# Kernel optimization log

Measured on AMD Instinct MI355X. Metric: run time of the kernel, lower is better.

Reference implementation:

```python
import jax, jax.numpy as jnp
import numpy as np

DIM = 1024
N_HEADS = 16
HEAD_DIM = DIM // N_HEADS
COND_DIM = 1024
MLP_RATIO = 4
B = 8
L = 1024  # per-sequence length (equal lengths -> T = B*L packed tokens)
T = B * L
EPS = 1e-5


def setup_inputs() -> dict:
    key = jax.random.key(0)
    ks = jax.random.split(key, 16)
    s = 0.02
    # rotary tables: [max_pos, head_dim//2]
    inv_freq = 1.0 / (10000.0 ** (jnp.arange(0, HEAD_DIM, 2, dtype=jnp.float32) / HEAD_DIM))
    t = jnp.arange(L, dtype=jnp.float32)
    freqs = t[:, None] * inv_freq[None, :]  # [L, HEAD_DIM//2]
    return {
        "x": jax.random.normal(ks[0], (T, DIM), jnp.float32),
        "lengths": jnp.full((B,), L, dtype=jnp.int64),
        "offsets": jnp.arange(B, dtype=jnp.int64) * L,
        "cos": jnp.cos(freqs),
        "sin": jnp.sin(freqs),
        "positions": jnp.tile(jnp.arange(L, dtype=jnp.int64), B),
        "c": jax.random.normal(ks[1], (B, COND_DIM), jnp.float32),
        "ln1_w": jnp.ones((DIM,), jnp.float32),
        "Wq": jax.random.normal(ks[2], (DIM, DIM), jnp.float32) * s,
        "Wk": jax.random.normal(ks[3], (DIM, DIM), jnp.float32) * s,
        "Wv": jax.random.normal(ks[4], (DIM, DIM), jnp.float32) * s,
        "Wo": jax.random.normal(ks[5], (DIM, DIM), jnp.float32) * s,
        "ln2_w": jnp.ones((DIM,), jnp.float32),
        "W1": jax.random.normal(ks[6], (DIM, MLP_RATIO * DIM), jnp.float32) * s,
        "b1": jnp.zeros((MLP_RATIO * DIM,), jnp.float32),
        "W2": jax.random.normal(ks[7], (MLP_RATIO * DIM, DIM), jnp.float32) * s,
        "b2": jnp.zeros((DIM,), jnp.float32),
        "ada_w": jax.random.normal(ks[8], (COND_DIM, 6 * DIM), jnp.float32) * s,
        "ada_b": jnp.zeros((6 * DIM,), jnp.float32),
    }


def _layer_norm(x, w):
    # LayerNorm with weight only (no bias), as in the torch module
    mu = jnp.mean(x, axis=-1, keepdims=True)
    var = jnp.mean(jnp.square(x - mu), axis=-1, keepdims=True)
    return (x - mu) * jax.lax.rsqrt(var + EPS) * w


def _rope(q, k, cos, sin, positions):
    # q, k: [T, H, D]; cos/sin: [max_pos, D//2]; half-split RoPE
    c = cos[positions][:, None, :]  # [T, 1, D//2]
    s = sin[positions][:, None, :]
    def rot(x):
        x1, x2 = jnp.split(x, 2, axis=-1)
        return jnp.concatenate([x1 * c - x2 * s, x2 * c + x1 * s], axis=-1)
    return rot(q), rot(k)


def reference(x, lengths, offsets, cos, sin, positions, c,
              ln1_w, Wq, Wk, Wv, Wo, ln2_w, W1, b1, W2, b2, ada_w, ada_b):
    # adaLN modulation: [B, 6*DIM] -> six [B, DIM]
    ada = c @ ada_w + ada_b
    sh_msa, sc_msa, g_msa, sh_mlp, sc_mlp, g_mlp = jnp.split(ada, 6, axis=-1)
    # per-token gather via seq_ids (equal lengths -> repeat each row L times)
    seq_ids = jnp.repeat(jnp.arange(B), L)  # = repeat_interleave(arange(B), lengths)
    sh_msa_t, sc_msa_t, g_msa_t = sh_msa[seq_ids], sc_msa[seq_ids], g_msa[seq_ids]
    sh_mlp_t, sc_mlp_t, g_mlp_t = sh_mlp[seq_ids], sc_mlp[seq_ids], g_mlp[seq_ids]

    x_skip = x
    h = _layer_norm(x, ln1_w) * (1.0 + sc_msa_t) + sh_msa_t
    q = (h @ Wq).reshape(T, N_HEADS, HEAD_DIM)
    k = (h @ Wk).reshape(T, N_HEADS, HEAD_DIM)
    v = (h @ Wv).reshape(T, N_HEADS, HEAD_DIM)
    q, k = _rope(q, k, cos, sin, positions)

    # intra-sequence-only attention: with equal lengths the block-diagonal
    # score_mod mask is exactly per-sequence attention -> reshape to [B, L, H, D]
    qb = q.reshape(B, L, N_HEADS, HEAD_DIM)
    kb = k.reshape(B, L, N_HEADS, HEAD_DIM)
    vb = v.reshape(B, L, N_HEADS, HEAD_DIM)
    scores = jnp.einsum('blhd,bmhd->bhlm', qb, kb) / jnp.sqrt(jnp.float32(HEAD_DIM))
    probs = jax.nn.softmax(scores, axis=-1)
    attn = jnp.einsum('bhlm,bmhd->blhd', probs, vb).reshape(T, DIM)

    x = x_skip + g_msa_t * (attn @ Wo)  # dropout p is identity in eval mode

    h2 = _layer_norm(x, ln2_w) * (1.0 + sc_mlp_t) + sh_mlp_t
    mlp = jax.nn.gelu(h2 @ W1 + b1, approximate=True) @ W2 + b2
    return x + g_mlp_t * mlp
```

## Files before the change

### kernel.cpp

```cpp
#include <hip/hip_runtime.h>

typedef unsigned short u16;
typedef __attribute__((ext_vector_type(8))) short short8;
typedef __attribute__((ext_vector_type(4))) float f32x4;
typedef __attribute__((ext_vector_type(4))) unsigned uint4v;

__device__ __forceinline__ float bf2f(u16 u){
  unsigned v = ((unsigned)u) << 16;
  return __builtin_bit_cast(float, v);
}
__device__ __forceinline__ u16 f2bf(float f){
  unsigned u = __builtin_bit_cast(unsigned, f);
  u += 0x7fff + ((u >> 16) & 1);
  return (u16)(u >> 16);
}
__device__ __forceinline__ unsigned packbf(float lo, float hi){
  return ((unsigned)f2bf(hi) << 16) | (unsigned)f2bf(lo);
}
__device__ __forceinline__ void async16(const void* g, void* l){
  __builtin_amdgcn_global_load_lds((const __attribute__((address_space(1))) void*)g,
                                   (__attribute__((address_space(3))) void*)l, 16, 0, 0);
}

__global__ __launch_bounds__(256) void ada_partial(
    const float* __restrict__ c, const float* __restrict__ aw,
    float* __restrict__ part){
  int n  = blockIdx.x*256 + threadIdx.x;
  int b  = blockIdx.y;
  int kc = blockIdx.z;
  const float* cr  = c + b*1024 + kc*128;
  const float* awp = aw + (size_t)(kc*128)*6144 + n;
  float acc = 0.f;
#pragma unroll 8
  for (int k = 0; k < 128; ++k)
    acc += cr[k] * awp[(size_t)k*6144];
  part[(size_t)(kc*8 + b)*6144 + n] = acc;
}

__global__ __launch_bounds__(256) void ada_reduce(
    const float* __restrict__ part, const float* __restrict__ ab,
    float* __restrict__ ada){
  int idx = blockIdx.x*256 + threadIdx.x;
  int n = idx % 6144;
  float acc = ab[n];
#pragma unroll
  for (int kc = 0; kc < 8; ++kc)
    acc += part[(size_t)kc*49152 + idx];
  ada[idx] = acc;
}

__global__ __launch_bounds__(256) void transpose_cast(
    const float* __restrict__ src, u16* __restrict__ dst, int K, int N){
  __shared__ float t[64][65];
  int n0 = blockIdx.x*64, k0 = blockIdx.y*64;
  int tid = threadIdx.x;
  int cc = tid & 63, r4 = tid >> 6;
#pragma unroll 4
  for (int it = 0; it < 16; ++it){
    int r = it*4 + r4;
    t[r][cc] = src[(size_t)(k0 + r)*N + n0 + cc];
  }
  __syncthreads();
#pragma unroll 4
  for (int it = 0; it < 16; ++it){
    int r = it*4 + r4;
    dst[(size_t)(n0 + r)*K + k0 + cc] = f2bf(t[cc][r]);
  }
}

__global__ __launch_bounds__(256) void ln_mod(
    const float* __restrict__ x, u16* __restrict__ out,
    const float* __restrict__ w, const float* __restrict__ ada,
    int shift_off, int scale_off){
  int t = blockIdx.x, tid = threadIdx.x;
  const float* xr = x + (size_t)t*1024;
  float v[4]; float s = 0.f, ss = 0.f;
#pragma unroll
  for (int i = 0; i < 4; ++i){ v[i] = xr[tid + i*256]; s += v[i]; ss += v[i]*v[i]; }
  for (int d = 1; d < 64; d <<= 1){ s += __shfl_xor(s, d); ss += __shfl_xor(ss, d); }
  __shared__ float red[8];
  int wv = tid >> 6;
  if ((tid & 63) == 0){ red[wv] = s; red[4+wv] = ss; }
  __syncthreads();
  s = red[0]+red[1]+red[2]+red[3];
  ss = red[4]+red[5]+red[6]+red[7];
  float mu = s * (1.f/1024.f);
  float var = ss * (1.f/1024.f) - mu*mu;
  float rs = rsqrtf(var + 1e-5f);
  int b = t >> 10;
  const float* sh = ada + b*6144 + shift_off;
  const float* sc = ada + b*6144 + scale_off;
#pragma unroll
  for (int i = 0; i < 4; ++i){
    int cidx = tid + i*256;
    float hh = (v[i]-mu)*rs*w[cidx]*(1.f + sc[cidx]) + sh[cidx];
    out[(size_t)t*1024 + cidx] = f2bf(hh);
  }
}

template<int EPI>
__global__ __launch_bounds__(256) void gemm_bt(
    const u16* __restrict__ A, const u16* __restrict__ Bt,
    void* __restrict__ Cout, int M, int N, int K, int m_off,
    const float* __restrict__ e0, const float* __restrict__ e1,
    const float* __restrict__ e2){
  __shared__ u16 As[128*32];
  __shared__ u16 Bs[128*32];
  const int tid = threadIdx.x;
  const int n0 = blockIdx.x*128, m0 = blockIdx.y*128;
  const int w = tid >> 6, lane = tid & 63, quad = lane >> 4, ln = lane & 15;
  const int wm = (w >> 1)*64, wn = (w & 1)*64;
  f32x4 acc[4][4] = {};
  const u16* ga = A  + (size_t)(m0 + (tid>>2))*K + (tid&3)*8;
  const u16* gb = Bt + (size_t)(n0 + (tid>>2))*K + (tid&3)*8;
  u16* lA = As + (tid & 192)*8;
  u16* lB = Bs + (tid & 192)*8;
  const size_t rstep = (size_t)64*K;
  for (int k0 = 0; k0 < K; k0 += 32){
    async16(ga,         lA);
    async16(ga + rstep, lA + 2048);
    async16(gb,         lB);
    async16(gb + rstep, lB + 2048);
    ga += 32; gb += 32;
    __syncthreads();
    short8 af[4], bfr[4];
#pragma unroll
    for (int i = 0; i < 4; ++i){
      af[i]  = *(const short8*)(As + (wm + i*16 + ln)*32 + quad*8);
      bfr[i] = *(const short8*)(Bs + (wn + i*16 + ln)*32 + quad*8);
    }
#pragma unroll
    for (int i = 0; i < 4; ++i)
#pragma unroll
      for (int j = 0; j < 4; ++j)
        acc[i][j] = __builtin_amdgcn_mfma_f32_16x16x32_bf16(af[i], bfr[j], acc[i][j], 0, 0, 0);
    __syncthreads();
  }
  const int mB = m0 + wm + quad*4;
  const int nB = n0 + wn + ln;
#pragma unroll
  for (int i = 0; i < 4; ++i){
#pragma unroll
    for (int r = 0; r < 4; ++r){
      const int m = mB + i*16 + r;
#pragma unroll
      for (int j = 0; j < 4; ++j){
        const int n = nB + j*16;
        float v = acc[i][j][r];
        if (EPI == 0){
          ((u16*)Cout)[(size_t)m*N + n] = f2bf(v);
        } else if (EPI == 1){
          const int b = (m + m_off) >> 10;
          float g = e1[b*6144 + 2048 + n];
          ((float*)Cout)[(size_t)m*N + n] = e0[(size_t)m*N + n] + g*v;
        } else if (EPI == 2){
          float xx = v + e0[n];
          float th = tanhf(0.7978845608f*(xx + 0.044715f*xx*xx*xx));
          ((u16*)Cout)[(size_t)m*N + n] = f2bf(0.5f*xx*(1.0f + th));
        } else {
          const int b = (m + m_off) >> 10;
          float g = e1[b*6144 + 5120 + n];
          ((float*)Cout)[(size_t)m*N + n] = e2[(size_t)m*N + n] + g*(v + e0[n]);
        }
      }
    }
  }
}

__global__ __launch_bounds__(256) void rope_pack(
    const u16* __restrict__ qkv, const float* __restrict__ cosT,
    const float* __restrict__ sinT, u16* __restrict__ qp,
    u16* __restrict__ kp, u16* __restrict__ vt){
  int blk = blockIdx.x;
  int lt = blk & 15, h = (blk >> 4) & 15, b = blk >> 8;
  int l0 = lt*64;
  int bh = b*16 + h;
  __shared__ u16 vl[64][68];
  int tid = threadIdx.x;
  size_t tile_base = (size_t)bh*65536 + (size_t)lt*4096;
#pragma unroll 4
  for (int it = 0; it < 16; ++it){
    int idx = it*256 + tid;
    int r = idx >> 6, d = idx & 63;
    int t = b*1024 + l0 + r;
    int pos = l0 + r;
    const u16* row = qkv + (size_t)t*3072 + h*64;
    float qv = bf2f(row[d]), kv = bf2f(row[1024+d]);
    float qo, ko;
    if (d < 32){
      float cs = cosT[pos*32 + d], sn = sinT[pos*32 + d];
      qo = qv*cs - bf2f(row[d+32])*sn;
      ko = kv*cs - bf2f(row[1024+d+32])*sn;
    } else {
      int dd = d - 32;
      float cs = cosT[pos*32 + dd], sn = sinT[pos*32 + dd];
      qo = qv*cs + bf2f(row[d-32])*sn;
      ko = kv*cs + bf2f(row[1024+d-32])*sn;
    }
    qp[((size_t)bh*1024 + l0 + r)*64 + d] = f2bf(qo*0.125f);
    kp[tile_base + (d>>5)*2048 + r*32 + (d&31)] = f2bf(ko);
    vl[d][r] = row[2048 + d];
  }
  __syncthreads();
#pragma unroll 4
  for (int it = 0; it < 16; ++it){
    int idx = it*256 + tid;
    int d = idx >> 6, cc = idx & 63;
    vt[tile_base + (cc>>5)*2048 + d*32 + (cc&31)] = vl[d][cc];
  }
}

__global__ __launch_bounds__(256) void attn_kernel(
    const u16* __restrict__ qp, const u16* __restrict__ kp,
    const u16* __restrict__ vtp, u16* __restrict__ ao){
  __shared__ u16 Kb[4096];
  __shared__ u16 Vb[4096];
  int tid = threadIdx.x, w = tid >> 6, lane = tid & 63;
  int quad = lane >> 4, ln = lane & 15;
  int bh = blockIdx.x >> 4, qb = blockIdx.x & 15;
  int h = bh & 15, b = bh >> 4;
  const u16* Q  = qp  + ((size_t)bh*1024 + qb*64 + w*16)*64;
  const u16* Kg = kp  + (size_t)bh*65536;
  const u16* Vg = vtp + (size_t)bh*65536;
  short8 qf0 = *(const short8*)(Q + ln*64 + quad*8);
  short8 qf1 = *(const short8*)(Q + ln*64 + 32 + quad*8);
  f32x4 o[4] = {};
  float m = -3e38f, l = 0.f;
  for (int kt = 0; kt < 16; ++kt){
    const u16* ktg = Kg + kt*4096 + lane*8;
    const u16* vtg = Vg + kt*4096 + lane*8;
    async16(ktg + (w*2+0)*512, Kb + (w*2+0)*512);
    async16(ktg + (w*2+1)*512, Kb + (w*2+1)*512);
    async16(vtg + (w*2+0)*512, Vb + (w*2+0)*512);
    async16(vtg + (w*2+1)*512, Vb + (w*2+1)*512);
    __syncthreads();
    f32x4 zz = {0.f, 0.f, 0.f, 0.f};
    f32x4 st[4];
#pragma unroll
    for (int c = 0; c < 4; ++c){
      short8 k0 = *(const short8*)(Kb +        (c*16 + ln)*32 + quad*8);
      short8 k1 = *(const short8*)(Kb + 2048 + (c*16 + ln)*32 + quad*8);
      st[c] = __builtin_amdgcn_mfma_f32_16x16x32_bf16(k0, qf0, zz, 0,0,0);
      st[c] = __builtin_amdgcn_mfma_f32_16x16x32_bf16(k1, qf1, st[c], 0,0,0);
    }
    short8 va[4][2];
#pragma unroll
    for (int dc = 0; dc < 4; ++dc)
#pragma unroll
      for (int kh = 0; kh < 2; ++kh)
        va[dc][kh] = *(const short8*)(Vb + kh*2048 + (dc*16 + ln)*32 + quad*8);
    float mx = st[0][0];
#pragma unroll
    for (int c = 0; c < 4; ++c)
#pragma unroll
      for (int r = 0; r < 4; ++r) mx = fmaxf(mx, st[c][r]);
    mx = fmaxf(mx, __shfl_xor(mx, 16));
    mx = fmaxf(mx, __shfl_xor(mx, 32));
    float mn = fmaxf(m, mx);
    float alpha = __expf(m - mn);
    m = mn;
    float p[4][4];
#pragma unroll
    for (int c = 0; c < 4; ++c)
#pragma unroll
      for (int r = 0; r < 4; ++r) p[c][r] = __expf(st[c][r] - mn);
    float sum = ((p[0][0]+p[0][1]) + (p[0][2]+p[0][3])) + ((p[1][0]+p[1][1]) + (p[1][2]+p[1][3]))
              + ((p[2][0]+p[2][1]) + (p[2][2]+p[2][3])) + ((p[3][0]+p[3][1]) + (p[3][2]+p[3][3]));
    sum += __shfl_xor(sum, 16);
    sum += __shfl_xor(sum, 32);
    l = l*alpha + sum;
#pragma unroll
    for (int dc = 0; dc < 4; ++dc)
#pragma unroll
      for (int r = 0; r < 4; ++r) o[dc][r] *= alpha;
    unsigned pc[4][2];
#pragma unroll
    for (int c = 0; c < 4; ++c){
      pc[c][0] = packbf(p[c][0], p[c][1]);
      pc[c][1] = packbf(p[c][2], p[c][3]);
    }
    const int sA = ((quad & 1)*2)*16 + ln;
    const int sB = sA + 16;
    const bool hi = quad >= 2;
#pragma unroll
    for (int kh = 0; kh < 2; ++kh){
      unsigned a0 = (unsigned)__shfl((int)pc[2*kh][0],   sA);
      unsigned b0 = (unsigned)__shfl((int)pc[2*kh+1][0], sA);
      unsigned a1 = (unsigned)__shfl((int)pc[2*kh][1],   sA);
      unsigned b1 = (unsigned)__shfl((int)pc[2*kh+1][1], sA);
      unsigned a2 = (unsigned)__shfl((int)pc[2*kh][0],   sB);
      unsigned b2 = (unsigned)__shfl((int)pc[2*kh+1][0], sB);
      unsigned a3 = (unsigned)__shfl((int)pc[2*kh][1],   sB);
      unsigned b3 = (unsigned)__shfl((int)pc[2*kh+1][1], sB);
      uint4v u = { hi ? b0 : a0, hi ? b1 : a1, hi ? b2 : a2, hi ? b3 : a3 };
      short8 pfrag = __builtin_bit_cast(short8, u);
#pragma unroll
      for (int dc = 0; dc < 4; ++dc)
        o[dc] = __builtin_amdgcn_mfma_f32_16x16x32_bf16(va[dc][kh], pfrag, o[dc], 0,0,0);
    }
    __syncthreads();
  }
  float rl = 1.f / l;
  size_t orow = ((size_t)b*1024 + qb*64 + w*16 + ln)*1024 + h*64;
#pragma unroll
  for (int dc = 0; dc < 4; ++dc)
#pragma unroll
    for (int r = 0; r < 4; ++r)
      ao[orow + dc*16 + quad*4 + r] = f2bf(o[dc][r] * rl);
}

extern "C" void kernel_launch(void* const* d_in, const int* in_sizes, int n_in,
                              void* d_out, int out_size, void* d_ws, size_t ws_size,
                              hipStream_t stream){
  const float* x    = (const float*)d_in[0];
  const float* cosT = (const float*)d_in[3];
  const float* sinT = (const float*)d_in[4];
  const float* c    = (const float*)d_in[6];
  const float* ln1w = (const float*)d_in[7];
  const float* Wq   = (const float*)d_in[8];
  const float* Wk   = (const float*)d_in[9];
  const float* Wv   = (const float*)d_in[10];
  const float* Wo   = (const float*)d_in[11];
  const float* ln2w = (const float*)d_in[12];
  const float* W1   = (const float*)d_in[13];
  const float* b1   = (const float*)d_in[14];
  const float* W2   = (const float*)d_in[15];
  const float* b2   = (const float*)d_in[16];
  const float* adaW = (const float*)d_in[17];
  const float* adaB = (const float*)d_in[18];

  char* ws = (char*)d_ws;
  float* ada  = (float*)(ws);
  u16* wqkvt  = (u16*)  (ws + 262144);
  u16* wot    = (u16*)  (ws + 6553600);
  u16* w1t    = (u16*)  (ws + 8650752);
  u16* w2t    = (u16*)  (ws + 17039360);
  u16* h      = (u16*)  (ws + 25427968);
  u16* qp     = (u16*)  (ws + 25427968);
  u16* h2     = (u16*)  (ws + 25427968);
  u16* qkv    = (u16*)  (ws + 42205184);
  u16* attnb  = (u16*)  (ws + 42205184);
  float* xmid = (float*)(ws + 58982400);
  float* adaP = (float*)(ws + 92536832);
  u16* kp     = (u16*)  (ws + 92536832);
  u16* vt     = (u16*)  (ws + 109314048);
  u16* hid    = (u16*)  (ws + 92536832);
  u16* hidF   = (u16*)  (ws + 126091264);
  float* out  = (float*)d_out;
  const bool bigws = ws_size >= (size_t)193200128;

  ada_partial<<<dim3(24,8,8), 256, 0, stream>>>(c, adaW, adaP);
  ada_reduce<<<192, 256, 0, stream>>>(adaP, adaB, ada);
  transpose_cast<<<dim3(16,16), 256, 0, stream>>>(Wq, wqkvt,             1024, 1024);
  transpose_cast<<<dim3(16,16), 256, 0, stream>>>(Wk, wqkvt + 1024*1024, 1024, 1024);
  transpose_cast<<<dim3(16,16), 256, 0, stream>>>(Wv, wqkvt + 2048*1024, 1024, 1024);
  transpose_cast<<<dim3(16,16), 256, 0, stream>>>(Wo, wot,               1024, 1024);
  transpose_cast<<<dim3(64,16), 256, 0, stream>>>(W1, w1t,               1024, 4096);
  transpose_cast<<<dim3(16,64), 256, 0, stream>>>(W2, w2t,               4096, 1024);
  ln_mod<<<8192, 256, 0, stream>>>(x, h, ln1w, ada, 0, 1024);
  gemm_bt<0><<<dim3(24,64), 256, 0, stream>>>(h, wqkvt, qkv, 8192, 3072, 1024, 0,
                                              nullptr, nullptr, nullptr);
  rope_pack<<<2048, 256, 0, stream>>>(qkv, cosT, sinT, qp, kp, vt);
  attn_kernel<<<2048, 256, 0, stream>>>(qp, kp, vt, attnb);
  gemm_bt<1><<<dim3(8,64), 256, 0, stream>>>(attnb, wot, xmid, 8192, 1024, 1024, 0,
                                             x, ada, nullptr);
  ln_mod<<<8192, 256, 0, stream>>>(xmid, h2, ln2w, ada, 3072, 4096);
  if (bigws){
    gemm_bt<2><<<dim3(32,64), 256, 0, stream>>>(h2, w1t, hidF, 8192, 4096, 1024, 0,
                                                b1, nullptr, nullptr);
    gemm_bt<3><<<dim3(8,64), 256, 0, stream>>>(hidF, w2t, out, 8192, 1024, 4096, 0,
                                               b2, ada, xmid);
  } else {
    for (int cch = 0; cch < 2; ++cch){
      const size_t mo = (size_t)cch*4096;
      gemm_bt<2><<<dim3(32,32), 256, 0, stream>>>(h2 + mo*1024, w1t, hid,
                                                  4096, 4096, 1024, (int)mo,
                                                  b1, nullptr, nullptr);
      gemm_bt<3><<<dim3(8,32), 256, 0, stream>>>(hid, w2t, out + mo*1024,
                                                 4096, 1024, 4096, (int)mo,
                                                 b2, ada, xmid + mo*1024);
    }
  }
}
```

Measured before the change: 661.3 us.

## Rewrite GEMM as 256x256 tile with 4-stage async LDS pipeline

```diff
diff --git a/kernel.cpp b/kernel.cpp
--- a/kernel.cpp
+++ b/kernel.cpp
@@ -21,6 +21,7 @@
   __builtin_amdgcn_global_load_lds((const __attribute__((address_space(1))) void*)g,
                                    (__attribute__((address_space(3))) void*)l, 16, 0, 0);
 }
+#define VMW(n) asm volatile("s_waitcnt vmcnt(" #n ")" ::: "memory")
 
 __global__ __launch_bounds__(256) void ada_partial(
     const float* __restrict__ c, const float* __restrict__ aw,
@@ -99,47 +100,86 @@
 }
 
 template<int EPI>
-__global__ __launch_bounds__(256) void gemm_bt(
+__global__ __launch_bounds__(512, 2) void gemm_bt(
     const u16* __restrict__ A, const u16* __restrict__ Bt,
     void* __restrict__ Cout, int M, int N, int K, int m_off,
     const float* __restrict__ e0, const float* __restrict__ e1,
     const float* __restrict__ e2){
-  __shared__ u16 As[128*32];
-  __shared__ u16 Bs[128*32];
+  __shared__ u16 lds[65536];
   const int tid = threadIdx.x;
-  const int n0 = blockIdx.x*128, m0 = blockIdx.y*128;
-  const int w = tid >> 6, lane = tid & 63, quad = lane >> 4, ln = lane & 15;
-  const int wm = (w >> 1)*64, wn = (w & 1)*64;
-  f32x4 acc[4][4] = {};
-  const u16* ga = A  + (size_t)(m0 + (tid>>2))*K + (tid&3)*8;
-  const u16* gb = Bt + (size_t)(n0 + (tid>>2))*K + (tid&3)*8;
-  u16* lA = As + (tid & 192)*8;
-  u16* lB = Bs + (tid & 192)*8;
-  const size_t rstep = (size_t)64*K;
-  for (int k0 = 0; k0 < K; k0 += 32){
-    async16(ga,         lA);
-    async16(ga + rstep, lA + 2048);
-    async16(gb,         lB);
-    async16(gb + rstep, lB + 2048);
-    ga += 32; gb += 32;
-    __syncthreads();
-    short8 af[4], bfr[4];
-#pragma unroll
-    for (int i = 0; i < 4; ++i){
-      af[i]  = *(const short8*)(As + (wm + i*16 + ln)*32 + quad*8);
-      bfr[i] = *(const short8*)(Bs + (wn + i*16 + ln)*32 + quad*8);
-    }
+  const int wv = tid >> 6, lane = tid & 63;
+  const int quad = lane >> 4, ln = lane & 15;
+  const int wr = wv >> 2, wc = wv & 3;
+  const int n0 = blockIdx.x*256, m0 = blockIdx.y*256;
+  const int nt = K >> 5;
+
+  const u16* Ap = A  + (size_t)(m0 + wv*16 + (lane>>2))*K + (lane&3)*8;
+  const u16* Bp = Bt + (size_t)(n0 + wv*16 + (lane>>2))*K + (lane&3)*8;
+  const size_t hstep = (size_t)128*K;
+  u16* lw = lds + wv*512;
+
+  f32x4 acc[8][4] = {};
+
+#pragma unroll
+  for (int tau = 0; tau < 3; ++tau){
+    u16* d = lw + tau*16384;
+    async16(Ap + (size_t)tau*32,         d);
+    async16(Ap + hstep + (size_t)tau*32, d + 4096);
+    async16(Bp + (size_t)tau*32,         d + 8192);
+    async16(Bp + hstep + (size_t)tau*32, d + 12288);
+  }
+  VMW(8);
+  __builtin_amdgcn_s_barrier();
+
+  const u16* Ar = lds + (wr*128 + ln)*32 + quad*8;
+  const u16* Br = lds + 8192 + (wc*64 + ln)*32 + quad*8;
+
+  for (int t = 0; t < nt; ++t){
+    const int bo = (t & 3)*16384;
+    short8 bfr[4], af[4];
+#pragma unroll
+    for (int j = 0; j < 4; ++j) bfr[j] = *(const short8*)(Br + bo + j*512);
+#pragma unroll
+    for (int i = 0; i < 4; ++i) af[i]  = *(const short8*)(Ar + bo + i*512);
+    if (t + 3 < nt){
+      u16* d = lw + ((t+3)&3)*16384;
+      async16(Ap + (size_t)(t+3)*32,         d);
+      async16(Ap + hstep + (size_t)(t+3)*32, d + 4096);
+    }
+    __builtin_amdgcn_s_barrier();
+    __builtin_amdgcn_s_setprio(1);
 #pragma unroll
     for (int i = 0; i < 4; ++i)
 #pragma unroll
       for (int j = 0; j < 4; ++j)
         acc[i][j] = __builtin_amdgcn_mfma_f32_16x16x32_bf16(af[i], bfr[j], acc[i][j], 0, 0, 0);
-    __syncthreads();
-  }
-  const int mB = m0 + wm + quad*4;
-  const int nB = n0 + wn + ln;
-#pragma unroll
-  for (int i = 0; i < 4; ++i){
+    __builtin_amdgcn_s_setprio(0);
+    __builtin_amdgcn_s_barrier();
+#pragma unroll
+    for (int i = 0; i < 4; ++i) af[i] = *(const short8*)(Ar + bo + 2048 + i*512);
+    if (t + 3 < nt){
+      u16* d = lw + ((t+3)&3)*16384;
+      async16(Bp + (size_t)(t+3)*32,         d + 8192);
+      async16(Bp + hstep + (size_t)(t+3)*32, d + 12288);
+    }
+    __builtin_amdgcn_s_barrier();
+    __builtin_amdgcn_s_setprio(1);
+#pragma unroll
+    for (int i = 0; i < 4; ++i)
+#pragma unroll
+      for (int j = 0; j < 4; ++j)
+        acc[4+i][j] = __builtin_amdgcn_mfma_f32_16x16x32_bf16(af[i], bfr[j], acc[4+i][j], 0, 0, 0);
+    __builtin_amdgcn_s_setprio(0);
+    if (t + 4 <= nt)      VMW(8);
+    else if (t + 3 == nt) VMW(4);
+    else if (t + 2 == nt) VMW(0);
+    __builtin_amdgcn_s_barrier();
+  }
+
+  const int mB = m0 + wr*128 + quad*4;
+  const int nB = n0 + wc*64 + ln;
+#pragma unroll
+  for (int i = 0; i < 8; ++i){
 #pragma unroll
     for (int r = 0; r < 4; ++r){
       const int m = mB + i*16 + r;
@@ -155,8 +195,8 @@
           ((float*)Cout)[(size_t)m*N + n] = e0[(size_t)m*N + n] + g*v;
         } else if (EPI == 2){
           float xx = v + e0[n];
-          float th = tanhf(0.7978845608f*(xx + 0.044715f*xx*xx*xx));
-          ((u16*)Cout)[(size_t)m*N + n] = f2bf(0.5f*xx*(1.0f + th));
+          float u = xx*(1.5957691216f + 0.07135481626f*xx*xx);
+          ((u16*)Cout)[(size_t)m*N + n] = f2bf(xx / (1.f + __expf(-u)));
         } else {
           const int b = (m + m_off) >> 10;
           float g = e1[b*6144 + 5120 + n];
@@ -358,25 +398,25 @@
   transpose_cast<<<dim3(64,16), 256, 0, stream>>>(W1, w1t,               1024, 4096);
   transpose_cast<<<dim3(16,64), 256, 0, stream>>>(W2, w2t,               4096, 1024);
   ln_mod<<<8192, 256, 0, stream>>>(x, h, ln1w, ada, 0, 1024);
-  gemm_bt<0><<<dim3(24,64), 256, 0, stream>>>(h, wqkvt, qkv, 8192, 3072, 1024, 0,
+  gemm_bt<0><<<dim3(12,32), 512, 0, stream>>>(h, wqkvt, qkv, 8192, 3072, 1024, 0,
                                               nullptr, nullptr, nullptr);
   rope_pack<<<2048, 256, 0, stream>>>(qkv, cosT, sinT, qp, kp, vt);
   attn_kernel<<<2048, 256, 0, stream>>>(qp, kp, vt, attnb);
-  gemm_bt<1><<<dim3(8,64), 256, 0, stream>>>(attnb, wot, xmid, 8192, 1024, 1024, 0,
+  gemm_bt<1><<<dim3(4,32), 512, 0, stream>>>(attnb, wot, xmid, 8192, 1024, 1024, 0,
                                              x, ada, nullptr);
   ln_mod<<<8192, 256, 0, stream>>>(xmid, h2, ln2w, ada, 3072, 4096);
   if (bigws){
-    gemm_bt<2><<<dim3(32,64), 256, 0, stream>>>(h2, w1t, hidF, 8192, 4096, 1024, 0,
+    gemm_bt<2><<<dim3(16,32), 512, 0, stream>>>(h2, w1t, hidF, 8192, 4096, 1024, 0,
                                                 b1, nullptr, nullptr);
-    gemm_bt<3><<<dim3(8,64), 256, 0, stream>>>(hidF, w2t, out, 8192, 1024, 4096, 0,
+    gemm_bt<3><<<dim3(4,32), 512, 0, stream>>>(hidF, w2t, out, 8192, 1024, 4096, 0,
                                                b2, ada, xmid);
   } else {
     for (int cch = 0; cch < 2; ++cch){
       const size_t mo = (size_t)cch*4096;
-      gemm_bt<2><<<dim3(32,32), 256, 0, stream>>>(h2 + mo*1024, w1t, hid,
+      gemm_bt<2><<<dim3(16,16), 512, 0, stream>>>(h2 + mo*1024, w1t, hid,
                                                   4096, 4096, 1024, (int)mo,
                                                   b1, nullptr, nullptr);
-      gemm_bt<3><<<dim3(8,32), 256, 0, stream>>>(hid, w2t, out + mo*1024,
+      gemm_bt<3><<<dim3(4,16), 512, 0, stream>>>(hid, w2t, out + mo*1024,
                                                  4096, 1024, 4096, (int)mo,
                                                  b2, ada, xmid + mo*1024);
     }
```

Result: no change. 664.2 us (+0.4%).
